# Optimization experiments

Measured on AMD Instinct MI355X. Metric: run time of the kernel, lower is better.

Reference implementation:

```python
import jax, jax.numpy as jnp
import numpy as np

# Batched-graph geometry: 128 graphs x 400 nodes x 6400 edges
N_GRAPHS = 128
NODES_PER = 400
EDGES_PER = 6400
N_NODES = N_GRAPHS * NODES_PER      # 51200
N_EDGES = N_GRAPHS * EDGES_PER      # 819200
F_IN = 256
HID = 64
K = 8          # num_filtrations
D = 3          # outputs per coordinate function (4 funs -> 12 total)


def coord_feats(p, t_tri, t_gau, sig, W_lin, b_lin, c_rh, r_rh):
    """Apply the 4 coordinate transforms to persistence pairs p: [K, M, 2].
    Returns [M, K*4D] with layout cat-over-coordfuns inside, cat-over-filtrations outside,
    matching torch: cat([cat([mod(p_k) for mod in funs],1) for k],1)."""
    x0, x1 = p[..., 0:1], p[..., 1:2]                       # [K,M,1]
    tri = jax.nn.relu(x1 - jnp.abs(t_tri - x0))             # Triangle_transform -> [K,M,D]
    d2 = jnp.sum((p[..., None, :] - t_gau) ** 2, axis=-1)   # [K,M,D]
    gau = jnp.exp(-d2 / (2.0 * sig[0] ** 2))                # Gaussian_transform
    lin = p @ W_lin + b_lin                                 # Line_transform
    l1 = jnp.abs(x0 - c_rh) + jnp.abs(x1 - c_rh)            # L1 dist to centers
    rh = 1.0 / (1.0 + l1) - 1.0 / (1.0 + jnp.abs(jnp.abs(r_rh[0]) - l1))  # RationalHat
    feats = jnp.concatenate([tri, gau, lin, rh], axis=-1)   # [K,M,4D]
    Kk, M, Dd = feats.shape
    return feats.transpose(1, 0, 2).reshape(M, Kk * Dd)     # [M, K*4D]


def setup_inputs() -> dict:
    key = jax.random.key(0)
    ks = jax.random.split(key, 24)
    x = jax.random.normal(ks[0], (N_NODES, F_IN), jnp.float32)
    # edges drawn within each graph block
    offs = (jnp.arange(N_EDGES) // EDGES_PER) * NODES_PER
    edge_index = jax.random.randint(ks[1], (2, N_EDGES), 0, NODES_PER) + offs[None, :]
    batch_vec = jnp.arange(N_NODES) // NODES_PER            # graph id per node
    edge_slices = jnp.arange(N_GRAPHS + 1) * EDGES_PER
    s = lambda i, shape: (jax.random.normal(ks[i], shape, jnp.float32) * 0.1)
    inp = dict(
        x=x, edge_index=edge_index, batch_vec=batch_vec, edge_slices=edge_slices,
        # shared filtration MLP: Linear(F_IN,HID)-ReLU-Linear(HID,K)-ReLU
        W1=s(2, (F_IN, HID)), b1=jnp.zeros((HID,), jnp.float32),
        W2=s(3, (HID, K)), b2=jnp.zeros((K,), jnp.float32),
        # dim-0 coordinate-function params
        t_tri0=s(4, (D,)), t_gau0=s(5, (D, 2)), sig0=jnp.ones((1,), jnp.float32),
        W_lin0=s(6, (2, D)), b_lin0=jnp.zeros((D,), jnp.float32),
        c_rh0=s(7, (D,)), r_rh0=jnp.ones((1,), jnp.float32),
        # dim-1 coordinate-function params
        t_tri1=s(8, (D,)), t_gau1=s(9, (D, 2)), sig1=jnp.ones((1,), jnp.float32),
        W_lin1=s(10, (2, D)), b_lin1=jnp.zeros((D,), jnp.float32),
        c_rh1=s(11, (D,)), r_rh1=jnp.ones((1,), jnp.float32),
        # output linear: in = F_IN + 2*K*4D (dist_dim1=True, non-residual path)
        W_out=s(12, (F_IN + 2 * K * 4 * D, F_IN)), b_out=jnp.zeros((F_IN,), jnp.float32),
    )
    return inp


def reference(x, edge_index, batch_vec, edge_slices,
              W1, b1, W2, b2,
              t_tri0, t_gau0, sig0, W_lin0, b_lin0, c_rh0, r_rh0,
              t_tri1, t_gau1, sig1, W_lin1, b_lin1, c_rh1, r_rh1,
              W_out, b_out):
    # per-node filtration values (shared params, relu_filtrations)
    fv = jax.nn.relu(jax.nn.relu(x @ W1 + b1) @ W2 + b2)            # [N,K]
    # edge filtration = max of endpoint values
    fe = jnp.maximum(fv[edge_index[0]], fv[edge_index[1]])          # [E,K]
    # fake dim-0 persistence: pairs (v, v) for every vertex, per filtration
    pers0 = jnp.broadcast_to(fv.T[..., None], (K, fv.shape[0], 2))  # [K,N,2]
    # fake dim-1: one unpaired tuple per graph = max edge value, placed at first edge
    eb = batch_vec[edge_index[0]]                                   # [E] graph id per edge
    unpaired = jax.ops.segment_max(fe, eb, num_segments=N_GRAPHS)   # [B,K]
    chosen = edge_slices[:-1]                                       # deterministic edge per graph
    pers1 = jnp.zeros((edge_index.shape[1], K, 2), fv.dtype)
    pers1 = pers1.at[chosen, :, 0].set(unpaired)
    pers1 = pers1.transpose(1, 0, 2)                                # [K,E,2]
    # coordinate-function activations
    act0 = coord_feats(pers0, t_tri0, t_gau0, sig0, W_lin0, b_lin0, c_rh0, r_rh0)  # [N, K*12]
    mask = jnp.any(pers1 != 0, axis=(0, 2))                         # [E]
    act1 = coord_feats(pers1, t_tri1, t_gau1, sig1, W_lin1, b_lin1, c_rh1, r_rh1)  # [E, K*12]
    g1 = jax.ops.segment_sum(act1 * mask[:, None].astype(act1.dtype), eb,
                             num_segments=N_GRAPHS)                 # [B, K*12]
    concat = jnp.concatenate([x, act0, g1[batch_vec]], axis=1)      # [N, F_IN + 2*K*12]
    return jax.nn.relu(concat @ W_out + b_out)                      # [N, F_IN]
```

## Files before the change

kernel.cpp:

```cpp
#include <hip/hip_runtime.h>

#define N_GRAPHS 128
#define NODES_PER 400
#define EDGES_PER 6400
#define N_NODES (N_GRAPHS * NODES_PER)
#define N_EDGES (N_GRAPHS * EDGES_PER)
#define F_IN 256
#define HID 64
#define FEAT 96
#define KTOT 352

typedef __attribute__((ext_vector_type(8))) short bf16x8;
typedef __attribute__((ext_vector_type(4))) float f32x4;

union u4b8 { uint4 u; bf16x8 v; };

__device__ __forceinline__ unsigned short f2b(float f) {
  union { float f; unsigned int u; } c; c.f = f;
  const unsigned int r = c.u + 0x7FFFu + ((c.u >> 16) & 1u);
  return (unsigned short)(r >> 16);
}

__device__ __forceinline__ float coord_one(
    int fun, int d, float x0, float x1,
    const float* __restrict__ t_tri, const float* __restrict__ t_gau,
    const float* __restrict__ sig, const float* __restrict__ W_lin,
    const float* __restrict__ b_lin, const float* __restrict__ c_rh,
    const float* __restrict__ r_rh) {
  if (fun == 0) {
    return fmaxf(x1 - fabsf(t_tri[d] - x0), 0.f);
  } else if (fun == 1) {
    const float dx = x0 - t_gau[d * 2 + 0];
    const float dy = x1 - t_gau[d * 2 + 1];
    const float s = sig[0];
    return expf(-(dx * dx + dy * dy) / (2.f * s * s));
  } else if (fun == 2) {
    return x0 * W_lin[d] + x1 * W_lin[3 + d] + b_lin[d];
  } else {
    const float l1 = fabsf(x0 - c_rh[d]) + fabsf(x1 - c_rh[d]);
    return 1.f / (1.f + l1) - 1.f / (1.f + fabsf(fabsf(r_rh[0]) - l1));
  }
}

__global__ __launch_bounds__(256) void k_wt(
    const float* __restrict__ W_out, const float* __restrict__ W1,
    unsigned short* __restrict__ Wt2, unsigned short* __restrict__ Wt1c) {
  const int idx = blockIdx.x * 256 + threadIdx.x;
  if (idx < KTOT * 256) {
    const int k = idx >> 8, c = idx & 255;
    Wt2[((size_t)(k >> 3) * 256 + c) * 8 + (k & 7)] = f2b(W_out[idx]);
  } else {
    const int j = idx - KTOT * 256;
    const int k = j >> 6, c = j & 63;
    Wt1c[((size_t)(k >> 3) * 64 + c) * 8 + (k & 7)] = f2b(W1[j]);
  }
}

__global__ __launch_bounds__(256, 3) void k_fv(
    const float* __restrict__ x, const unsigned short* __restrict__ Wt1c,
    const float* __restrict__ b1, const float* __restrict__ W2,
    const float* __restrict__ b2,
    const float* __restrict__ t_tri, const float* __restrict__ t_gau,
    const float* __restrict__ sig, const float* __restrict__ W_lin,
    const float* __restrict__ b_lin, const float* __restrict__ c_rh,
    const float* __restrict__ r_rh,
    float* __restrict__ fv, unsigned short* __restrict__ ext,
    unsigned short* __restrict__ xb, const int write_xb) {
  __shared__ float W2s[HID * 8];
  __shared__ float Hs[4][16][68];
  const int tid = threadIdx.x;
  const int wave = tid >> 6, lane = tid & 63;
  const int l15 = lane & 15, l4 = lane >> 4;
  const int n0 = blockIdx.x * 64;

  W2s[tid] = W2[tid];
  W2s[tid + 256] = W2[tid + 256];
  __syncthreads();

  const int arow = n0 + wave * 16 + l15;
  bf16x8 afr[8];
  #pragma unroll
  for (int kt = 0; kt < 8; ++kt) {
    const size_t go = (size_t)arow * F_IN + kt * 32 + l4 * 8;
    const float4 f0 = *(const float4*)&x[go];
    const float4 f1 = *(const float4*)&x[go + 4];
    u4b8 w;
    w.u.x = (unsigned)f2b(f0.x) | ((unsigned)f2b(f0.y) << 16);
    w.u.y = (unsigned)f2b(f0.z) | ((unsigned)f2b(f0.w) << 16);
    w.u.z = (unsigned)f2b(f1.x) | ((unsigned)f2b(f1.y) << 16);
    w.u.w = (unsigned)f2b(f1.z) | ((unsigned)f2b(f1.w) << 16);
    if (write_xb) *(uint4*)&xb[go] = w.u;
    afr[kt] = w.v;
  }

  f32x4 acc[4];
  #pragma unroll
  for (int nf = 0; nf < 4; ++nf) acc[nf] = (f32x4){0.f, 0.f, 0.f, 0.f};
  #pragma unroll
  for (int kt = 0; kt < 8; ++kt) {
    const unsigned short* wb = Wt1c + (size_t)(kt * 4 + l4) * 512;
    #pragma unroll
    for (int nf = 0; nf < 4; ++nf) {
      const bf16x8 b = *(const bf16x8*)&wb[(nf * 16 + l15) * 8];
      acc[nf] = __builtin_amdgcn_mfma_f32_16x16x32_bf16(afr[kt], b, acc[nf], 0, 0, 0);
    }
  }

  #pragma unroll
  for (int nf = 0; nf < 4; ++nf) {
    const int col = nf * 16 + l15;
    const float bb = b1[col];
    #pragma unroll
    for (int j = 0; j < 4; ++j)
      Hs[wave][l4 * 4 + j][col] = fmaxf(acc[nf][j] + bb, 0.f);
  }
  __syncthreads();

  #pragma unroll
  for (int p = tid; p < 512; p += 256) {
    const int row = p >> 3, kk = p & 7;
    const float* hr = Hs[row >> 4][row & 15];
    float s = b2[kk];
    #pragma unroll 8
    for (int j = 0; j < HID; ++j) s = fmaf(hr[j], W2s[j * 8 + kk], s);
    s = fmaxf(s, 0.f);
    const int n = n0 + row;
    fv[(size_t)n * 8 + kk] = s;

    unsigned short o[12] __attribute__((aligned(16)));
    #pragma unroll
    for (int fun = 0; fun < 4; ++fun)
      #pragma unroll
      for (int d = 0; d < 3; ++d)
        o[fun * 3 + d] = f2b(coord_one(fun, d, s, s,
                             t_tri, t_gau, sig, W_lin, b_lin, c_rh, r_rh));
    unsigned short* dst = &ext[(size_t)n * FEAT + kk * 12];
    *(uint2*)&dst[0] = *(const uint2*)&o[0];
    *(uint2*)&dst[4] = *(const uint2*)&o[4];
    *(uint2*)&dst[8] = *(const uint2*)&o[8];
  }
}

#define CHUNK (EDGES_PER / 8)
__global__ __launch_bounds__(256) void k_unpaired(
    const int* __restrict__ ei, const float* __restrict__ fv,
    float* __restrict__ unpP) {
  __shared__ float lfv[NODES_PER * 8];
  __shared__ float red[256][8];
  const int g = blockIdx.x >> 3, ch = blockIdx.x & 7;
  const int tid = threadIdx.x;

  for (int i = tid; i < NODES_PER * 2; i += 256)
    *(float4*)&lfv[i * 4] = *(const float4*)&fv[(size_t)g * NODES_PER * 8 + i * 4];
  __syncthreads();

  float lm[8];
  #pragma unroll
  for (int k = 0; k < 8; ++k) lm[k] = 0.f;
  const int e0 = g * EDGES_PER + ch * CHUNK;
  for (int e = e0 + tid; e < e0 + CHUNK; e += 256) {
    const int a = ei[e] - g * NODES_PER;
    const int b = ei[N_EDGES + e] - g * NODES_PER;
    const float4 a0 = *(const float4*)&lfv[a * 8];
    const float4 a1 = *(const float4*)&lfv[a * 8 + 4];
    const float4 b0 = *(const float4*)&lfv[b * 8];
    const float4 b1 = *(const float4*)&lfv[b * 8 + 4];
    lm[0] = fmaxf(lm[0], fmaxf(a0.x, b0.x));
    lm[1] = fmaxf(lm[1], fmaxf(a0.y, b0.y));
    lm[2] = fmaxf(lm[2], fmaxf(a0.z, b0.z));
    lm[3] = fmaxf(lm[3], fmaxf(a0.w, b0.w));
    lm[4] = fmaxf(lm[4], fmaxf(a1.x, b1.x));
    lm[5] = fmaxf(lm[5], fmaxf(a1.y, b1.y));
    lm[6] = fmaxf(lm[6], fmaxf(a1.z, b1.z));
    lm[7] = fmaxf(lm[7], fmaxf(a1.w, b1.w));
  }
  #pragma unroll
  for (int k = 0; k < 8; ++k) red[tid][k] = lm[k];
  __syncthreads();
  for (int s = 128; s > 0; s >>= 1) {
    if (tid < s) {
      #pragma unroll
      for (int k = 0; k < 8; ++k)
        red[tid][k] = fmaxf(red[tid][k], red[tid + s][k]);
    }
    __syncthreads();
  }
  if (tid < 8) unpP[(size_t)(g * 8 + ch) * 8 + tid] = red[0][tid];
}

__global__ __launch_bounds__(256) void k_g1G(
    const float* __restrict__ unpP, const float* __restrict__ t_tri,
    const float* __restrict__ t_gau, const float* __restrict__ sig,
    const float* __restrict__ W_lin, const float* __restrict__ b_lin,
    const float* __restrict__ c_rh, const float* __restrict__ r_rh,
    const float* __restrict__ W_out, const float* __restrict__ b_out,
    float* __restrict__ G) {
  const int g = blockIdx.x;
  const int t = threadIdx.x;
  __shared__ float u[8];
  __shared__ float feat[96];
  if (t < 8) {
    float m = 0.f;
    #pragma unroll
    for (int ch = 0; ch < 8; ++ch)
      m = fmaxf(m, unpP[(size_t)(g * 8 + ch) * 8 + t]);
    u[t] = m;
  }
  __syncthreads();
  if (t < 96) {
    const float mask = (u[0] != 0.f || u[1] != 0.f || u[2] != 0.f ||
                        u[3] != 0.f || u[4] != 0.f || u[5] != 0.f ||
                        u[6] != 0.f || u[7] != 0.f) ? 1.f : 0.f;
    const int k = t / 12;
    const int fun = (t % 12) / 3;
    const int d = t % 3;
    feat[t] = mask * coord_one(fun, d, u[k], 0.f,
                               t_tri, t_gau, sig, W_lin, b_lin, c_rh, r_rh);
  }
  __syncthreads();
  float s = b_out[t];
  #pragma unroll 4
  for (int f = 0; f < 96; ++f)
    s = fmaf(feat[f], W_out[(size_t)(352 + f) * 256 + t], s);
  G[g * 256 + t] = s;
}

__global__ __launch_bounds__(256, 2) void k_out_mfma(
    const float* __restrict__ x, const unsigned short* __restrict__ xb,
    const unsigned short* __restrict__ ext,
    const unsigned short* __restrict__ Wt2, const float* __restrict__ G,
    float* __restrict__ out, const int use_xb) {
  const int tid = threadIdx.x;
  const int wave = tid >> 6, lane = tid & 63;
  const int l15 = lane & 15, l4 = lane >> 4;
  const int q = wave;

  bf16x8 b[11][4];
  #pragma unroll
  for (int ks = 0; ks < 11; ++ks)
    #pragma unroll
    for (int nf = 0; nf < 4; ++nf)
      b[ks][nf] = *(const bf16x8*)
          &Wt2[((size_t)(ks * 4 + l4) * 256 + q * 64 + nf * 16 + l15) * 8];

  for (int t = blockIdx.x; t < N_NODES / 16; t += gridDim.x) {
    const int arow = t * 16 + l15;
    const int gidx = t / 25;

    bf16x8 a[11];
    if (use_xb) {
      #pragma unroll
      for (int ks = 0; ks < 8; ++ks)
        a[ks] = *(const bf16x8*)&xb[(size_t)arow * F_IN + ks * 32 + l4 * 8];
    } else {
      #pragma unroll
      for (int ks = 0; ks < 8; ++ks) {
        const size_t go = (size_t)arow * F_IN + ks * 32 + l4 * 8;
        const float4 f0 = *(const float4*)&x[go];
        const float4 f1 = *(const float4*)&x[go + 4];
        u4b8 w;
        w.u.x = (unsigned)f2b(f0.x) | ((unsigned)f2b(f0.y) << 16);
        w.u.y = (unsigned)f2b(f0.z) | ((unsigned)f2b(f0.w) << 16);
        w.u.z = (unsigned)f2b(f1.x) | ((unsigned)f2b(f1.y) << 16);
        w.u.w = (unsigned)f2b(f1.z) | ((unsigned)f2b(f1.w) << 16);
        a[ks] = w.v;
      }
    }
    #pragma unroll
    for (int ks = 8; ks < 11; ++ks)
      a[ks] = *(const bf16x8*)&ext[(size_t)arow * FEAT + (ks - 8) * 32 + l4 * 8];

    f32x4 acc[4];
    #pragma unroll
    for (int nf = 0; nf < 4; ++nf) acc[nf] = (f32x4){0.f, 0.f, 0.f, 0.f};
    #pragma unroll
    for (int ks = 0; ks < 11; ++ks)
      #pragma unroll
      for (int nf = 0; nf < 4; ++nf)
        acc[nf] = __builtin_amdgcn_mfma_f32_16x16x32_bf16(
            a[ks], b[ks][nf], acc[nf], 0, 0, 0);

    #pragma unroll
    for (int nf = 0; nf < 4; ++nf) {
      const int col = q * 64 + nf * 16 + l15;
      const float gv = G[gidx * 256 + col];
      #pragma unroll
      for (int j = 0; j < 4; ++j) {
        const int row = t * 16 + l4 * 4 + j;
        out[(size_t)row * 256 + col] = fmaxf(acc[nf][j] + gv, 0.f);
      }
    }
  }
}

extern "C" void kernel_launch(void* const* d_in, const int* in_sizes, int n_in,
                              void* d_out, int out_size, void* d_ws, size_t ws_size,
                              hipStream_t stream) {
  const float* x          = (const float*)d_in[0];
  const int*   edge_index = (const int*)d_in[1];
  const float* W1     = (const float*)d_in[4];
  const float* b1     = (const float*)d_in[5];
  const float* W2     = (const float*)d_in[6];
  const float* b2     = (const float*)d_in[7];
  const float* t_tri0 = (const float*)d_in[8];
  const float* t_gau0 = (const float*)d_in[9];
  const float* sig0   = (const float*)d_in[10];
  const float* W_lin0 = (const float*)d_in[11];
  const float* b_lin0 = (const float*)d_in[12];
  const float* c_rh0  = (const float*)d_in[13];
  const float* r_rh0  = (const float*)d_in[14];
  const float* t_tri1 = (const float*)d_in[15];
  const float* t_gau1 = (const float*)d_in[16];
  const float* sig1   = (const float*)d_in[17];
  const float* W_lin1 = (const float*)d_in[18];
  const float* b_lin1 = (const float*)d_in[19];
  const float* c_rh1  = (const float*)d_in[20];
  const float* r_rh1  = (const float*)d_in[21];
  const float* W_out  = (const float*)d_in[22];
  const float* b_out  = (const float*)d_in[23];
  float* out = (float*)d_out;

  char* base = (char*)d_ws;
  float* fv            = (float*)(base + 0);
  float* unpP          = (float*)(base + 1638400);
  float* G             = (float*)(base + 1671168);
  unsigned short* Wt2  = (unsigned short*)(base + 1802240);
  unsigned short* Wt1c = (unsigned short*)(base + 1982464);
  unsigned short* ext  = (unsigned short*)(base + 2015232);
  unsigned short* xb   = (unsigned short*)(base + 11845632);
  const size_t ws_need_xb = 11845632 + (size_t)N_NODES * F_IN * 2;
  const int use_xb = ws_size >= ws_need_xb ? 1 : 0;

  k_wt<<<(KTOT * 256 + F_IN * HID) / 256, 256, 0, stream>>>(W_out, W1, Wt2, Wt1c);
  k_fv<<<N_NODES / 64, 256, 0, stream>>>(
      x, Wt1c, b1, W2, b2,
      t_tri0, t_gau0, sig0, W_lin0, b_lin0, c_rh0, r_rh0,
      fv, ext, xb, use_xb);
  k_unpaired<<<N_GRAPHS * 8, 256, 0, stream>>>(edge_index, fv, unpP);
  k_g1G<<<N_GRAPHS, 256, 0, stream>>>(unpP, t_tri1, t_gau1, sig1,
                                      W_lin1, b_lin1, c_rh1, r_rh1,
                                      W_out, b_out, G);
  k_out_mfma<<<512, 256, 0, stream>>>(x, xb, ext, Wt2, G, out, use_xb);
}
```

Measured before the change: 73.34 us.

## Split output GEMM across 8 waves and use hardware bf16 packing

```diff
diff --git a/kernel.cpp b/kernel.cpp
--- a/kernel.cpp
+++ b/kernel.cpp
@@ -1,4 +1,5 @@
 #include <hip/hip_runtime.h>
+#include <hip/hip_bf16.h>
 
 #define N_GRAPHS 128
 #define NODES_PER 400
@@ -19,6 +20,11 @@
   union { float f; unsigned int u; } c; c.f = f;
   const unsigned int r = c.u + 0x7FFFu + ((c.u >> 16) & 1u);
   return (unsigned short)(r >> 16);
+}
+
+__device__ __forceinline__ unsigned pkbf2(float lo, float hi) {
+  __hip_bfloat162 h = __float22bfloat162_rn(make_float2(lo, hi));
+  return *reinterpret_cast<unsigned*>(&h);
 }
 
 __device__ __forceinline__ float coord_one(
@@ -85,10 +91,10 @@
     const float4 f0 = *(const float4*)&x[go];
     const float4 f1 = *(const float4*)&x[go + 4];
     u4b8 w;
-    w.u.x = (unsigned)f2b(f0.x) | ((unsigned)f2b(f0.y) << 16);
-    w.u.y = (unsigned)f2b(f0.z) | ((unsigned)f2b(f0.w) << 16);
-    w.u.z = (unsigned)f2b(f1.x) | ((unsigned)f2b(f1.y) << 16);
-    w.u.w = (unsigned)f2b(f1.z) | ((unsigned)f2b(f1.w) << 16);
+    w.u.x = pkbf2(f0.x, f0.y);
+    w.u.y = pkbf2(f0.z, f0.w);
+    w.u.z = pkbf2(f1.x, f1.y);
+    w.u.w = pkbf2(f1.z, f1.w);
     if (write_xb) *(uint4*)&xb[go] = w.u;
     afr[kt] = w.v;
   }
@@ -127,17 +133,20 @@
     const int n = n0 + row;
     fv[(size_t)n * 8 + kk] = s;
 
-    unsigned short o[12] __attribute__((aligned(16)));
+    float fo[12];
     #pragma unroll
     for (int fun = 0; fun < 4; ++fun)
       #pragma unroll
       for (int d = 0; d < 3; ++d)
-        o[fun * 3 + d] = f2b(coord_one(fun, d, s, s,
-                             t_tri, t_gau, sig, W_lin, b_lin, c_rh, r_rh));
+        fo[fun * 3 + d] = coord_one(fun, d, s, s,
+                                    t_tri, t_gau, sig, W_lin, b_lin, c_rh, r_rh);
+    unsigned o32[6];
+    #pragma unroll
+    for (int i = 0; i < 6; ++i) o32[i] = pkbf2(fo[2 * i], fo[2 * i + 1]);
     unsigned short* dst = &ext[(size_t)n * FEAT + kk * 12];
-    *(uint2*)&dst[0] = *(const uint2*)&o[0];
-    *(uint2*)&dst[4] = *(const uint2*)&o[4];
-    *(uint2*)&dst[8] = *(const uint2*)&o[8];
+    *(uint2*)&dst[0] = make_uint2(o32[0], o32[1]);
+    *(uint2*)&dst[4] = make_uint2(o32[2], o32[3]);
+    *(uint2*)&dst[8] = make_uint2(o32[4], o32[5]);
   }
 }
 
@@ -225,7 +234,7 @@
   G[g * 256 + t] = s;
 }
 
-__global__ __launch_bounds__(256, 2) void k_out_mfma(
+__global__ __launch_bounds__(512, 4) void k_out_mfma(
     const float* __restrict__ x, const unsigned short* __restrict__ xb,
     const unsigned short* __restrict__ ext,
     const unsigned short* __restrict__ Wt2, const float* __restrict__ G,
@@ -233,56 +242,58 @@
   const int tid = threadIdx.x;
   const int wave = tid >> 6, lane = tid & 63;
   const int l15 = lane & 15, l4 = lane >> 4;
-  const int q = wave;
-
-  bf16x8 b[11][4];
+  const int c0 = wave * 32;
+
+  bf16x8 b[11][2];
   #pragma unroll
   for (int ks = 0; ks < 11; ++ks)
     #pragma unroll
-    for (int nf = 0; nf < 4; ++nf)
+    for (int nf = 0; nf < 2; ++nf)
       b[ks][nf] = *(const bf16x8*)
-          &Wt2[((size_t)(ks * 4 + l4) * 256 + q * 64 + nf * 16 + l15) * 8];
+          &Wt2[((size_t)(ks * 4 + l4) * 256 + c0 + nf * 16 + l15) * 8];
 
   for (int t = blockIdx.x; t < N_NODES / 16; t += gridDim.x) {
     const int arow = t * 16 + l15;
     const int gidx = t / 25;
 
-    bf16x8 a[11];
+    f32x4 acc[2];
+    acc[0] = (f32x4){0.f, 0.f, 0.f, 0.f};
+    acc[1] = (f32x4){0.f, 0.f, 0.f, 0.f};
+
     if (use_xb) {
       #pragma unroll
-      for (int ks = 0; ks < 8; ++ks)
-        a[ks] = *(const bf16x8*)&xb[(size_t)arow * F_IN + ks * 32 + l4 * 8];
+      for (int ks = 0; ks < 11; ++ks) {
+        const bf16x8 a = (ks < 8)
+            ? *(const bf16x8*)&xb[(size_t)arow * F_IN + ks * 32 + l4 * 8]
+            : *(const bf16x8*)&ext[(size_t)arow * FEAT + (ks - 8) * 32 + l4 * 8];
+        acc[0] = __builtin_amdgcn_mfma_f32_16x16x32_bf16(a, b[ks][0], acc[0], 0, 0, 0);
+        acc[1] = __builtin_amdgcn_mfma_f32_16x16x32_bf16(a, b[ks][1], acc[1], 0, 0, 0);
+      }
     } else {
       #pragma unroll
-      for (int ks = 0; ks < 8; ++ks) {
-        const size_t go = (size_t)arow * F_IN + ks * 32 + l4 * 8;
-        const float4 f0 = *(const float4*)&x[go];
-        const float4 f1 = *(const float4*)&x[go + 4];
-        u4b8 w;
-        w.u.x = (unsigned)f2b(f0.x) | ((unsigned)f2b(f0.y) << 16);
-        w.u.y = (unsigned)f2b(f0.z) | ((unsigned)f2b(f0.w) << 16);
-        w.u.z = (unsigned)f2b(f1.x) | ((unsigned)f2b(f1.y) << 16);
-        w.u.w = (unsigned)f2b(f1.z) | ((unsigned)f2b(f1.w) << 16);
-        a[ks] = w.v;
+      for (int ks = 0; ks < 11; ++ks) {
+        bf16x8 a;
+        if (ks < 8) {
+          const size_t go = (size_t)arow * F_IN + ks * 32 + l4 * 8;
+          const float4 f0 = *(const float4*)&x[go];
+          const float4 f1 = *(const float4*)&x[go + 4];
+          u4b8 w;
+          w.u.x = pkbf2(f0.x, f0.y);
+          w.u.y = pkbf2(f0.z, f0.w);
+          w.u.z = pkbf2(f1.x, f1.y);
+          w.u.w = pkbf2(f1.z, f1.w);
+          a = w.v;
+        } else {
+          a = *(const bf16x8*)&ext[(size_t)arow * FEAT + (ks - 8) * 32 + l4 * 8];
+        }
+        acc[0] = __builtin_amdgcn_mfma_f32_16x16x32_bf16(a, b[ks][0], acc[0], 0, 0, 0);
+        acc[1] = __builtin_amdgcn_mfma_f32_16x16x32_bf16(a, b[ks][1], acc[1], 0, 0, 0);
       }
     }
-    #pragma unroll
-    for (int ks = 8; ks < 11; ++ks)
-      a[ks] = *(const bf16x8*)&ext[(size_t)arow * FEAT + (ks - 8) * 32 + l4 * 8];
-
-    f32x4 acc[4];
-    #pragma unroll
-    for (int nf = 0; nf < 4; ++nf) acc[nf] = (f32x4){0.f, 0.f, 0.f, 0.f};
-    #pragma unroll
-    for (int ks = 0; ks < 11; ++ks)
-      #pragma unroll
-      for (int nf = 0; nf < 4; ++nf)
-        acc[nf] = __builtin_amdgcn_mfma_f32_16x16x32_bf16(
-            a[ks], b[ks][nf], acc[nf], 0, 0, 0);
-
-    #pragma unroll
-    for (int nf = 0; nf < 4; ++nf) {
-      const int col = q * 64 + nf * 16 + l15;
+
+    #pragma unroll
+    for (int nf = 0; nf < 2; ++nf) {
+      const int col = c0 + nf * 16 + l15;
       const float gv = G[gidx * 256 + col];
       #pragma unroll
       for (int j = 0; j < 4; ++j) {
@@ -340,5 +351,5 @@
   k_g1G<<<N_GRAPHS, 256, 0, stream>>>(unpP, t_tri1, t_gau1, sig1,
                                       W_lin1, b_lin1, c_rh1, r_rh1,
                                       W_out, b_out, G);
-  k_out_mfma<<<512, 256, 0, stream>>>(x, xb, ext, Wt2, G, out, use_xb);
-}
+  k_out_mfma<<<512, 512, 0, stream>>>(x, xb, ext, Wt2, G, out, use_xb);
+}
```

Measured after the change: 86.23 us. +17.6%, slower.
